# Kernel optimization log

Hardware: AMD Instinct MI355X
Metric: run time of the kernel (lower is better)

## Reference

```python
import jax, jax.numpy as jnp
import numpy as np

NUM_GENES = 50000
NUM_EDGES = 5000
NNZ = 1_600_000
NUM_PATHWAYS = 500
NUM_TREATMENTS = 20
D = 128        # embed_dim
LATENT = 128   # latent_dim
B, M = 64, 200


def setup_inputs() -> dict:
    key = jax.random.key(0)
    ks = jax.random.split(key, 14)
    gene_ids = jax.random.randint(ks[0], (B, M), 0, NUM_GENES)
    context_ids = jax.random.randint(ks[1], (B,), 0, NUM_TREATMENTS)
    # sparse incidence H (COO): H[row, col] = val, shape [NUM_GENES, NUM_EDGES]
    H_rows = jax.random.randint(ks[2], (NNZ,), 0, NUM_GENES)
    H_cols = jax.random.randint(ks[3], (NNZ,), 0, NUM_EDGES)
    H_vals = jnp.ones((NNZ,), jnp.float32)
    gene_embed = 0.02 * jax.random.normal(ks[4], (NUM_GENES, D), jnp.float32)
    treatment_embed = 0.02 * jax.random.normal(ks[5], (NUM_TREATMENTS, D), jnp.float32)
    gene_pathway = jax.random.bernoulli(ks[6], 0.05, (NUM_GENES, NUM_PATHWAYS)).astype(jnp.float32)
    s = 1.0 / np.sqrt(2 * D)
    W1 = s * jax.random.normal(ks[7], (2 * D, D), jnp.float32)
    b1 = jnp.zeros((D,), jnp.float32)
    W2 = (1.0 / np.sqrt(D)) * jax.random.normal(ks[8], (D,), jnp.float32)
    b2 = jnp.zeros((), jnp.float32)
    latent_W = (1.0 / np.sqrt(D)) * jax.random.normal(ks[9], (D, LATENT), jnp.float32)
    latent_b = jnp.zeros((LATENT,), jnp.float32)
    risk_W = (1.0 / np.sqrt(LATENT)) * jax.random.normal(ks[10], (LATENT,), jnp.float32)
    risk_b = jnp.zeros((), jnp.float32)
    return dict(gene_ids=gene_ids, context_ids=context_ids, H_rows=H_rows, H_cols=H_cols,
                H_vals=H_vals, gene_embed=gene_embed, treatment_embed=treatment_embed,
                gene_pathway=gene_pathway, W1=W1, b1=b1, W2=W2, b2=b2,
                latent_W=latent_W, latent_b=latent_b, risk_W=risk_W, risk_b=risk_b)


def _hyper_prop(E, H_rows, H_cols, H_vals):
    Dv = jax.ops.segment_sum(H_vals, H_rows, num_segments=NUM_GENES)
    De = jax.ops.segment_sum(H_vals, H_cols, num_segments=NUM_EDGES)
    dv = jnp.power(Dv + 1e-6, -0.5)[:, None]   # [V,1]
    de = jnp.power(De + 1e-6, -1.0)[:, None]   # [E,1]
    X = E * dv
    # H^T X : scatter node rows into hyperedges
    HX = jax.ops.segment_sum(H_vals[:, None] * X[H_rows], H_cols, num_segments=NUM_EDGES)
    HX = HX * de
    # H (De^-1 H^T X)
    Xp = jax.ops.segment_sum(H_vals[:, None] * HX[H_cols], H_rows, num_segments=NUM_GENES)
    return Xp * dv


def reference(gene_ids, context_ids, H_rows, H_cols, H_vals, gene_embed, treatment_embed,
              gene_pathway, W1, b1, W2, b2, latent_W, latent_b, risk_W, risk_b):
    E_prop = _hyper_prop(gene_embed, H_rows, H_cols, H_vals)   # [V,D]
    X = E_prop[gene_ids]                                       # [B,M,D]
    ctx = treatment_embed[context_ids]                         # [B,D]
    masks = gene_pathway[gene_ids]                             # [B,M,P]
    pathway_sum = jnp.einsum('bmd,bmp->bpd', X, masks)         # [B,P,D]
    counts = jnp.clip(masks.sum(axis=1), 1.0)[..., None]       # [B,P,1]
    rep = pathway_sum / counts                                 # [B,P,D]
    ctx_exp = jnp.broadcast_to(ctx[:, None, :], (rep.shape[0], NUM_PATHWAYS, D))
    attn_in = jnp.concatenate([rep, ctx_exp], axis=-1)         # [B,P,2D]
    h = jnp.tanh(attn_in @ W1 + b1)                            # [B,P,D]
    scores = h @ W2 + b2                                       # [B,P]
    w = jax.nn.softmax(scores, axis=-1)
    z0 = jnp.einsum('bp,bpd->bd', w, rep)                      # [B,D]
    z = z0 @ latent_W + latent_b                               # [B,LATENT]
    risk = z @ risk_W + risk_b                                 # [B]
    return risk, z
```

## Files before the change

### kernel.cpp

```cpp
#include <hip/hip_runtime.h>
#include <math.h>

#define NGENES 50000
#define NEDGES 5000
#define NNZ_C 1600000
#define NPATH 500
#define DIM 128
#define BB 64
#define MM 200
#define BMN (BB * MM)
#define NBMW 1568
#define CSRCAP 400000
#define NCH 128
#define CHUNK (NNZ_C / NCH)
#define RNG 12512
#define GSTRIDE 50048
#define NT 8
#define TILESZ 6250
#define NBIN (NT * NEDGES)
#define BIN0 50048
#define RED_N 90048
#define SCB_BIN 40
#define SCB_ROW 49
#define SCB (SCB_BIN + SCB_ROW)


__device__ inline float wred_sum(float x) {
#pragma unroll
  for (int off = 32; off > 0; off >>= 1) x += __shfl_down(x, off, 64);
  return x;
}
__device__ inline int wred_sumi(int x) {
#pragma unroll
  for (int off = 32; off > 0; off >>= 1) x += __shfl_down(x, off, 64);
  return x;
}
__device__ inline float wred_max(float x) {
#pragma unroll
  for (int off = 32; off > 0; off >>= 1) x = fmaxf(x, __shfl_down(x, off, 64));
  return x;
}
__device__ inline int wave_incl_scan(int x) {
  int lane = threadIdx.x & 63;
#pragma unroll
  for (int off = 1; off < 64; off <<= 1) {
    int y = __shfl_up(x, off, 64);
    if (lane >= off) x += y;
  }
  return x;
}

__global__ void k_mark(const int* __restrict__ gene_ids, unsigned* __restrict__ bitmap) {
  int i = blockIdx.x * blockDim.x + threadIdx.x;
  if (i >= BMN) return;
  int g = gene_ids[i];
  atomicOr(bitmap + (g >> 5), 1u << (g & 31));
}

__global__ void k_build(const int* __restrict__ rows, const int* __restrict__ cols,
                        unsigned char* __restrict__ pgc, unsigned char* __restrict__ pbc) {
  __shared__ int hs[RNG];
  int c = blockIdx.x, role = blockIdx.y, tid = threadIdx.x;
  int lo = c * CHUNK, hi = lo + CHUNK;
  if (role == 0) {
    for (int j = tid; j < RNG; j += 1024) hs[j] = 0;
    __syncthreads();
    for (int i = lo + tid; i < hi; i += 1024) {
      int r = rows[i];
      int k = r / RNG;
      int j = r - k * RNG;
      atomicAdd(&hs[j], 1 << (k * 8));
    }
    __syncthreads();
    unsigned char* dst = pgc + (size_t)c * GSTRIDE;
    for (int j = tid; j < RNG; j += 1024) {
      unsigned v = (unsigned)hs[j];
      dst[j] = (unsigned char)(v & 0xFFu);
      dst[j + RNG] = (unsigned char)((v >> 8) & 0xFFu);
      dst[j + 2 * RNG] = (unsigned char)((v >> 16) & 0xFFu);
      dst[j + 3 * RNG] = (unsigned char)(v >> 24);
    }
  } else {
    for (int j = tid; j < 2 * NEDGES; j += 1024) hs[j] = 0;
    __syncthreads();
    for (int i = lo + tid; i < hi; i += 1024) {
      int r = rows[i];
      int t = r / TILESZ;
      int e = cols[i];
      atomicAdd(&hs[(t >> 2) * NEDGES + e], 1 << ((t & 3) * 8));
    }
    __syncthreads();
    unsigned char* dst = pbc + (size_t)c * NBIN;
    for (int j = tid; j < 2 * NEDGES; j += 1024) {
      int h = j / NEDGES, e = j - h * NEDGES;
      unsigned v = (unsigned)hs[j];
      int t0 = h * 4;
      dst[(size_t)(t0 + 0) * NEDGES + e] = (unsigned char)(v & 0xFFu);
      dst[(size_t)(t0 + 1) * NEDGES + e] = (unsigned char)((v >> 8) & 0xFFu);
      dst[(size_t)(t0 + 2) * NEDGES + e] = (unsigned char)((v >> 16) & 0xFFu);
      dst[(size_t)(t0 + 3) * NEDGES + e] = (unsigned char)(v >> 24);
    }
  }
}

__global__ void k_reduce(const unsigned char* __restrict__ pgc,
                         const unsigned char* __restrict__ pbc,
                         const unsigned* __restrict__ bitmap,
                         float* __restrict__ dv_inv, int* __restrict__ row_cnt,
                         unsigned short* __restrict__ ccpre8, int* __restrict__ cnt8em) {
  int idx = blockIdx.x * 256 + threadIdx.x;
  if (idx < NGENES) {
    int s = 0;
    for (int c = 0; c < NCH; ++c) s += pgc[(size_t)c * GSTRIDE + idx];
    dv_inv[idx] = 1.f / sqrtf((float)s + 1e-6f);
    row_cnt[idx] = ((bitmap[idx >> 5] >> (idx & 31)) & 1) ? s : 0;
  } else if (idx >= BIN0 && idx < BIN0 + NBIN) {
    int b = idx - BIN0;
    int t = b / NEDGES, e = b - t * NEDGES;
    int run = 0;
    for (int c = 0; c < NCH; ++c) {
      ccpre8[(size_t)c * NBIN + b] = (unsigned short)run;
      run += pbc[(size_t)c * NBIN + b];
    }
    cnt8em[(e << 3) | t] = run;
  }
}

__global__ void k_sc1(const int* __restrict__ cnt8em, const int* __restrict__ row_cnt,
                      int* __restrict__ bsum) {
  __shared__ int wsum[4];
  int blk = blockIdx.x, t = threadIdx.x, lane = t & 63, wid = t >> 6;
  const int* in;
  int base, n;
  if (blk < SCB_BIN) { in = cnt8em; base = blk * 1024; n = NBIN; }
  else { in = row_cnt; base = (blk - SCB_BIN) * 1024; n = NGENES; }
  int s = 0;
#pragma unroll
  for (int k = 0; k < 4; ++k) {
    int e = base + t + k * 256;
    if (e < n) s += in[e];
  }
  s = wred_sumi(s);
  if (lane == 0) wsum[wid] = s;
  __syncthreads();
  if (t == 0) bsum[blk] = wsum[0] + wsum[1] + wsum[2] + wsum[3];
}

__global__ void k_sc2(const int* __restrict__ bsum, int* __restrict__ boff) {
  int t = threadIdx.x, lane = t & 63, wid = t >> 6;
  if (wid == 0) {
    int x = (lane < SCB_BIN) ? bsum[lane] : 0;
    int incl = wave_incl_scan(x);
    if (lane < SCB_BIN) boff[lane] = incl - x;
  } else {
    int x = (lane < SCB_ROW) ? bsum[SCB_BIN + lane] : 0;
    int incl = wave_incl_scan(x);
    if (lane < SCB_ROW) boff[SCB_BIN + lane] = incl - x;
  }
}

__global__ void k_sc3(const int* __restrict__ cnt8em, const int* __restrict__ row_cnt,
                      const int* __restrict__ boff,
                      int* __restrict__ start8, int* __restrict__ row_start,
                      float* __restrict__ de_inv) {
  __shared__ int lds[1024];
  __shared__ int wsum[4];
  int blk = blockIdx.x, t = threadIdx.x, lane = t & 63, wid = t >> 6;
  const int* in;
  int* out;
  int base, n;
  if (blk < SCB_BIN) { in = cnt8em; out = start8; base = blk * 1024; n = NBIN; }
  else { in = row_cnt; out = row_start; base = (blk - SCB_BIN) * 1024; n = NGENES; }
  int coff = boff[blk];
#pragma unroll
  for (int k = 0; k < 4; ++k) {
    int e = t + k * 256;
    lds[e] = (base + e < n) ? in[base + e] : 0;
  }
  __syncthreads();
  int x0 = lds[4 * t], x1 = lds[4 * t + 1], x2 = lds[4 * t + 2], x3 = lds[4 * t + 3];
  int s = x0 + x1 + x2 + x3;
  int incl = wave_incl_scan(s);
  if (lane == 63) wsum[wid] = incl;
  __syncthreads();
  int woff = 0;
  for (int w = 0; w < wid; ++w) woff += wsum[w];
  int tb = coff + woff + incl - s;
  int i0 = base + 4 * t;
  if (i0 + 3 < n) {
    ((int4*)(out + i0))[0] = make_int4(tb, tb + x0, tb + x0 + x1, tb + x0 + x1 + x2);
  } else {
    if (i0 < n) out[i0] = tb;
    if (i0 + 1 < n) out[i0 + 1] = tb + x0;
    if (i0 + 2 < n) out[i0 + 2] = tb + x0 + x1;
    if (i0 + 3 < n) out[i0 + 3] = tb + x0 + x1 + x2;
  }
  if (blk < SCB_BIN && t < 128) {
    int e = blk * 128 + t;
    if (e < NEDGES) {
      int s8 = 0;
#pragma unroll
      for (int u = 0; u < 8; ++u) s8 += lds[8 * t + u];
      de_inv[e] = 1.f / ((float)s8 + 1e-6f);
    }
  }
}

__global__ void k_place(const int* __restrict__ rows, const int* __restrict__ cols,
                        const int* __restrict__ start8, const unsigned short* __restrict__ ccpre8,
                        const int* __restrict__ row_start, int* __restrict__ row_cur,
                        const unsigned* __restrict__ bitmap,
                        unsigned short* __restrict__ csc, unsigned short* __restrict__ csr) {
  __shared__ int cnt_s[NEDGES];
  __shared__ unsigned bm_s[NBMW];
  int c = blockIdx.x, q = blockIdx.y, tid = threadIdx.x;
  int lo = c * CHUNK, hi = lo + CHUNK;
  for (int j = tid; j < NEDGES; j += 1024) cnt_s[j] = 0;
  for (int j = tid; j < NBMW; j += 1024) bm_s[j] = bitmap[j];
  __syncthreads();
  const unsigned short* cp = ccpre8 + (size_t)c * NBIN;
  int qlo = q * (4 * TILESZ);
  for (int i = lo + tid; i < hi; i += 1024) {
    int r = rows[i];
    unsigned d = (unsigned)(r - qlo);
    if (d >= 4u * TILESZ) continue;
    int e = cols[i];
    int tt = (int)(d / (unsigned)TILESZ);
    int t = 4 * q + tt;
    int sh = tt * 8;
    int old = atomicAdd(&cnt_s[e], 1 << sh);
    int rank = (old >> sh) & 0xFF;
    int pos = start8[e * 8 + t] + (int)cp[(size_t)t * NEDGES + e] + rank;
    csc[pos] = (unsigned short)(d - (unsigned)(tt * TILESZ));
    if ((bm_s[r >> 5] >> (r & 31)) & 1) {
      int p2 = row_start[r] + atomicAdd(row_cur + r, 1);
      if (p2 < CSRCAP) csr[p2] = (unsigned short)e;
    }
  }
}

__global__ void k_edge_t(const int* __restrict__ start8, const int* __restrict__ cnt8em,
                         const unsigned short* __restrict__ csc,
                         const float* __restrict__ dv_inv, const float* __restrict__ ge,
                         float* __restrict__ part) {
  __shared__ float4 red[32];
  int bid = blockIdx.x;
  int s = start8[bid];
  int n = cnt8em[bid];
  int rbase = (bid & 7) * TILESZ;
  int g = threadIdx.x >> 5, l = threadIdx.x & 31;
  float4 a0 = make_float4(0.f, 0.f, 0.f, 0.f);
  float4 a1 = make_float4(0.f, 0.f, 0.f, 0.f);
  float4 a2 = make_float4(0.f, 0.f, 0.f, 0.f);
  float4 a3 = make_float4(0.f, 0.f, 0.f, 0.f);
  int i = s + g;
  int end = s + n;
  unsigned short c0 = 0, c1 = 0, c2 = 0, c3 = 0, c4 = 0, c5 = 0, c6 = 0, c7 = 0;
  bool have = (i + 14 < end);
  if (have) {
    c0 = csc[i];      c1 = csc[i + 2];  c2 = csc[i + 4];  c3 = csc[i + 6];
    c4 = csc[i + 8];  c5 = csc[i + 10]; c6 = csc[i + 12]; c7 = csc[i + 14];
  }
  while (have) {
    int ni = i + 16;
    bool nhave = (ni + 14 < end);
    unsigned short n0 = c0, n1 = c1, n2 = c2, n3 = c3, n4 = c4, n5 = c5, n6 = c6, n7 = c7;
    if (nhave) {
      n0 = csc[ni];      n1 = csc[ni + 2];  n2 = csc[ni + 4];  n3 = csc[ni + 6];
      n4 = csc[ni + 8];  n5 = csc[ni + 10]; n6 = csc[ni + 12]; n7 = csc[ni + 14];
    }
    int r0 = rbase + c0, r1 = rbase + c1, r2 = rbase + c2, r3 = rbase + c3;
    int r4 = rbase + c4, r5 = rbase + c5, r6 = rbase + c6, r7 = rbase + c7;
    float w0 = dv_inv[r0], w1 = dv_inv[r1], w2 = dv_inv[r2], w3 = dv_inv[r3];
    float w4 = dv_inv[r4], w5 = dv_inv[r5], w6 = dv_inv[r6], w7 = dv_inv[r7];
    float4 x0 = *((const float4*)(ge + (size_t)r0 * DIM) + l);
    float4 x1 = *((const float4*)(ge + (size_t)r1 * DIM) + l);
    float4 x2 = *((const float4*)(ge + (size_t)r2 * DIM) + l);
    float4 x3 = *((const float4*)(ge + (size_t)r3 * DIM) + l);
    float4 x4 = *((const float4*)(ge + (size_t)r4 * DIM) + l);
    float4 x5 = *((const float4*)(ge + (size_t)r5 * DIM) + l);
    float4 x6 = *((const float4*)(ge + (size_t)r6 * DIM) + l);
    float4 x7 = *((const float4*)(ge + (size_t)r7 * DIM) + l);
    a0.x += w0 * x0.x; a0.y += w0 * x0.y; a0.z += w0 * x0.z; a0.w += w0 * x0.w;
    a1.x += w1 * x1.x; a1.y += w1 * x1.y; a1.z += w1 * x1.z; a1.w += w1 * x1.w;
    a2.x += w2 * x2.x; a2.y += w2 * x2.y; a2.z += w2 * x2.z; a2.w += w2 * x2.w;
    a3.x += w3 * x3.x; a3.y += w3 * x3.y; a3.z += w3 * x3.z; a3.w += w3 * x3.w;
    a0.x += w4 * x4.x; a0.y += w4 * x4.y; a0.z += w4 * x4.z; a0.w += w4 * x4.w;
    a1.x += w5 * x5.x; a1.y += w5 * x5.y; a1.z += w5 * x5.z; a1.w += w5 * x5.w;
    a2.x += w6 * x6.x; a2.y += w6 * x6.y; a2.z += w6 * x6.z; a2.w += w6 * x6.w;
    a3.x += w7 * x7.x; a3.y += w7 * x7.y; a3.z += w7 * x7.z; a3.w += w7 * x7.w;
    c0 = n0; c1 = n1; c2 = n2; c3 = n3; c4 = n4; c5 = n5; c6 = n6; c7 = n7;
    i = ni;
    have = nhave;
  }
  for (; i + 2 < end; i += 4) {
    int ra = rbase + csc[i], rb = rbase + csc[i + 2];
    float wa = dv_inv[ra], wb = dv_inv[rb];
    float4 xa = *((const float4*)(ge + (size_t)ra * DIM) + l);
    float4 xb = *((const float4*)(ge + (size_t)rb * DIM) + l);
    a0.x += wa * xa.x; a0.y += wa * xa.y; a0.z += wa * xa.z; a0.w += wa * xa.w;
    a1.x += wb * xb.x; a1.y += wb * xb.y; a1.z += wb * xb.z; a1.w += wb * xb.w;
  }
  for (; i < end; i += 2) {
    int r = rbase + csc[i];
    float w = dv_inv[r];
    float4 x = *((const float4*)(ge + (size_t)r * DIM) + l);
    a0.x += w * x.x; a0.y += w * x.y; a0.z += w * x.z; a0.w += w * x.w;
  }
  a0.x += a1.x + a2.x + a3.x;
  a0.y += a1.y + a2.y + a3.y;
  a0.z += a1.z + a2.z + a3.z;
  a0.w += a1.w + a2.w + a3.w;
  if (g == 1) red[l] = a0;
  __syncthreads();
  if (g == 0) {
    float4 b = red[l];
    a0.x += b.x; a0.y += b.y; a0.z += b.z; a0.w += b.w;
    *((float4*)(part + (size_t)bid * DIM) + l) = a0;
  }
}

__global__ void k_edge_red(const float* __restrict__ part, const float* __restrict__ de_inv,
                           float* __restrict__ HXde) {
  int e = blockIdx.x, d = threadIdx.x;
  float s = 0.f;
#pragma unroll
  for (int t = 0; t < NT; ++t) s += part[((size_t)e * 8 + t) * DIM + d];
  HXde[(size_t)e * DIM + d] = s * de_inv[e];
}

__global__ void k_gene(const int* __restrict__ gene_ids, const int* __restrict__ row_start,
                       const int* __restrict__ row_cnt, const unsigned short* __restrict__ csr,
                       const float* __restrict__ HXde, const float* __restrict__ dv_inv,
                       float* __restrict__ Xg) {
  __shared__ float4 red[4][32];
  int bm = blockIdx.x;
  int gene = gene_ids[bm];
  int s = row_start[gene], n = row_cnt[gene];
  int end = s + n;
  int g = threadIdx.x >> 5, l = threadIdx.x & 31;
  float4 a0 = make_float4(0.f, 0.f, 0.f, 0.f);
  float4 a1 = make_float4(0.f, 0.f, 0.f, 0.f);
  int i = s + g;
  for (; i + 12 < end; i += 16) {
    int e0 = csr[i];
    int e1 = csr[i + 4];
    int e2 = csr[i + 8];
    int e3 = csr[i + 12];
    float4 x0 = *((const float4*)(HXde + (size_t)e0 * DIM) + l);
    float4 x1 = *((const float4*)(HXde + (size_t)e1 * DIM) + l);
    float4 x2 = *((const float4*)(HXde + (size_t)e2 * DIM) + l);
    float4 x3 = *((const float4*)(HXde + (size_t)e3 * DIM) + l);
    a0.x += x0.x; a0.y += x0.y; a0.z += x0.z; a0.w += x0.w;
    a1.x += x1.x; a1.y += x1.y; a1.z += x1.z; a1.w += x1.w;
    a0.x += x2.x; a0.y += x2.y; a0.z += x2.z; a0.w += x2.w;
    a1.x += x3.x; a1.y += x3.y; a1.z += x3.z; a1.w += x3.w;
  }
  for (; i + 4 < end; i += 8) {
    int e0 = csr[i];
    int e1 = csr[i + 4];
    float4 x0 = *((const float4*)(HXde + (size_t)e0 * DIM) + l);
    float4 x1 = *((const float4*)(HXde + (size_t)e1 * DIM) + l);
    a0.x += x0.x; a0.y += x0.y; a0.z += x0.z; a0.w += x0.w;
    a1.x += x1.x; a1.y += x1.y; a1.z += x1.z; a1.w += x1.w;
  }
  for (; i < end; i += 4) {
    int e0 = csr[i];
    float4 x = *((const float4*)(HXde + (size_t)e0 * DIM) + l);
    a0.x += x.x; a0.y += x.y; a0.z += x.z; a0.w += x.w;
  }
  a0.x += a1.x; a0.y += a1.y; a0.z += a1.z; a0.w += a1.w;
  red[g][l] = a0;
  __syncthreads();
  if (g == 0) {
    float4 a = red[0][l], b = red[1][l], c = red[2][l], d = red[3][l];
    float dvg = dv_inv[gene];
    float4 o;
    o.x = (a.x + b.x + c.x + d.x) * dvg;
    o.y = (a.y + b.y + c.y + d.y) * dvg;
    o.z = (a.z + b.z + c.z + d.z) * dvg;
    o.w = (a.w + b.w + c.w + d.w) * dvg;
    *((float4*)(Xg + (size_t)bm * DIM) + l) = o;
  }
}

#define PT 20
#define CHM 25
__global__ void k_pathway(const int* __restrict__ gene_ids,
                          const float* __restrict__ gene_pathway,
                          const float* __restrict__ Xg, float* __restrict__ rep) {
  __shared__ __align__(16) float buf[2][CHM * PT];
  __shared__ int gid_s[MM];
  int b = blockIdx.y;
  int p0 = blockIdx.x * PT;
  int t = threadIdx.x;
  int d = t;
  if (t < 128) gid_s[t] = gene_ids[b * MM + t];
  if (t + 128 < MM) gid_s[t + 128] = gene_ids[b * MM + t + 128];
  __syncthreads();
  float acc[PT], cnt[PT];
#pragma unroll
  for (int pp = 0; pp < PT; ++pp) { acc[pp] = 0.f; cnt[pp] = 0.f; }
  float r[4];
#pragma unroll
  for (int k = 0; k < 4; ++k) {
    int e = t + k * 128;
    if (e < CHM * PT) {
      int ml = e / PT, po = e - ml * PT;
      r[k] = gene_pathway[(size_t)gid_s[ml] * NPATH + p0 + po];
    }
  }
  const float* Xb = Xg + (size_t)b * MM * DIM + d;
  for (int ch = 0; ch < MM / CHM; ++ch) {
    float* bw = buf[ch & 1];
#pragma unroll
    for (int k = 0; k < 4; ++k) {
      int e = t + k * 128;
      if (e < CHM * PT) bw[e] = r[k];
    }
    __syncthreads();
    if (ch + 1 < MM / CHM) {
      int m0n = (ch + 1) * CHM;
#pragma unroll
      for (int k = 0; k < 4; ++k) {
        int e = t + k * 128;
        if (e < CHM * PT) {
          int ml = e / PT, po = e - ml * PT;
          r[k] = gene_pathway[(size_t)gid_s[m0n + ml] * NPATH + p0 + po];
        }
      }
    }
    const float* br = buf[ch & 1];
    int m0 = ch * CHM;
    for (int ml = 0; ml < CHM; ++ml) {
      float x = Xb[(size_t)(m0 + ml) * DIM];
      const float4* mr = (const float4*)(br + ml * PT);
#pragma unroll
      for (int q = 0; q < 5; ++q) {
        float4 v = mr[q];
        acc[4 * q + 0] += v.x * x; cnt[4 * q + 0] += v.x;
        acc[4 * q + 1] += v.y * x; cnt[4 * q + 1] += v.y;
        acc[4 * q + 2] += v.z * x; cnt[4 * q + 2] += v.z;
        acc[4 * q + 3] += v.w * x; cnt[4 * q + 3] += v.w;
      }
    }
  }
#pragma unroll
  for (int pp = 0; pp < PT; ++pp) {
    rep[((size_t)b * NPATH + p0 + pp) * DIM + d] = acc[pp] / fmaxf(cnt[pp], 1.f);
  }
}

#define PT2 10
__global__ void k_attn(const float* __restrict__ rep, const int* __restrict__ context_ids,
                       const float* __restrict__ treatment_embed,
                       const float* __restrict__ W1, const float* __restrict__ b1,
                       const float* __restrict__ W2, const float* __restrict__ b2,
                       float* __restrict__ scores) {
  __shared__ float in_s[PT2][DIM];
  __shared__ float ctx_s[DIM];
  __shared__ float part[PT2][2];
  int b = blockIdx.y;
  int p0 = blockIdx.x * PT2;
  int j = threadIdx.x;
  int lane = j & 63, wid = j >> 6;
  ctx_s[j] = treatment_embed[context_ids[b] * DIM + j];
#pragma unroll
  for (int pp = 0; pp < PT2; ++pp)
    in_s[pp][j] = rep[((size_t)b * NPATH + p0 + pp) * DIM + j];
  __syncthreads();
  float base = b1[j];
  for (int k = 0; k < DIM; ++k) base += ctx_s[k] * W1[(DIM + k) * DIM + j];
  float acc[PT2];
#pragma unroll
  for (int pp = 0; pp < PT2; ++pp) acc[pp] = base;
  for (int k = 0; k < DIM; ++k) {
    float w1 = W1[k * DIM + j];
#pragma unroll
    for (int pp = 0; pp < PT2; ++pp) acc[pp] += in_s[pp][k] * w1;
  }
  float w2 = W2[j];
#pragma unroll
  for (int pp = 0; pp < PT2; ++pp) {
    float t = tanhf(acc[pp]) * w2;
    t = wred_sum(t);
    if (lane == 0) part[pp][wid] = t;
  }
  __syncthreads();
  if (j < PT2) scores[b * NPATH + p0 + j] = part[j][0] + part[j][1] + b2[0];
}

__global__ void k_final(const float* __restrict__ scores, const float* __restrict__ rep,
                        const float* __restrict__ latent_W, const float* __restrict__ latent_b,
                        const float* __restrict__ risk_W, const float* __restrict__ risk_b,
                        float* __restrict__ out) {
  __shared__ float w_s[NPATH];
  __shared__ float z0_s[DIM];
  __shared__ float red_max[2], red_sum[2], red_risk[2];
  int b = blockIdx.x, t = threadIdx.x;
  int lane = t & 63, wid = t >> 6;
  float lmax = -3.4e38f;
  for (int p = t; p < NPATH; p += 128) {
    float s = scores[b * NPATH + p];
    w_s[p] = s;
    lmax = fmaxf(lmax, s);
  }
  lmax = wred_max(lmax);
  if (lane == 0) red_max[wid] = lmax;
  __syncthreads();
  float bmax = fmaxf(red_max[0], red_max[1]);
  float lsum = 0.f;
  for (int p = t; p < NPATH; p += 128) {
    float e = expf(w_s[p] - bmax);
    w_s[p] = e;
    lsum += e;
  }
  lsum = wred_sum(lsum);
  if (lane == 0) red_sum[wid] = lsum;
  __syncthreads();
  float inv = 1.f / (red_sum[0] + red_sum[1]);
  int d = t;
  const float* repb = rep + (size_t)b * NPATH * DIM + d;
  float z00 = 0.f, z01 = 0.f, z02 = 0.f, z03 = 0.f;
  for (int p = 0; p < NPATH; p += 4) {
    z00 += w_s[p] * repb[(size_t)p * DIM];
    z01 += w_s[p + 1] * repb[(size_t)(p + 1) * DIM];
    z02 += w_s[p + 2] * repb[(size_t)(p + 2) * DIM];
    z03 += w_s[p + 3] * repb[(size_t)(p + 3) * DIM];
  }
  float z0 = ((z00 + z01) + (z02 + z03)) * inv;
  z0_s[d] = z0;
  __syncthreads();
  float z = latent_b[t];
  for (int dd = 0; dd < DIM; ++dd) z += z0_s[dd] * latent_W[dd * DIM + t];
  out[BB + b * DIM + t] = z;
  float r = z * risk_W[t];
  r = wred_sum(r);
  if (lane == 0) red_risk[wid] = r;
  __syncthreads();
  if (t == 0) out[b] = red_risk[0] + red_risk[1] + risk_b[0];
}

extern "C" void kernel_launch(void* const* d_in, const int* in_sizes, int n_in,
                              void* d_out, int out_size, void* d_ws, size_t ws_size,
                              hipStream_t stream) {
  const int* gene_ids = (const int*)d_in[0];
  const int* context_ids = (const int*)d_in[1];
  const int* H_rows = (const int*)d_in[2];
  const int* H_cols = (const int*)d_in[3];
  const float* gene_embed = (const float*)d_in[5];
  const float* treatment_embed = (const float*)d_in[6];
  const float* gene_pathway = (const float*)d_in[7];
  const float* W1 = (const float*)d_in[8];
  const float* b1 = (const float*)d_in[9];
  const float* W2 = (const float*)d_in[10];
  const float* b2 = (const float*)d_in[11];
  const float* latent_W = (const float*)d_in[12];
  const float* latent_b = (const float*)d_in[13];
  const float* risk_W = (const float*)d_in[14];
  const float* risk_b = (const float*)d_in[15];
  float* out = (float*)d_out;

  char* ws = (char*)d_ws;
  float* dv_inv = (float*)(ws + 0);
  float* de_inv = (float*)(ws + 200000);
  int* row_cnt = (int*)(ws + 220000);
  int* row_start = (int*)(ws + 420000);
  int* cnt8em = (int*)(ws + 620000);
  int* start8 = (int*)(ws + 780000);
  float* scores = (float*)(ws + 940000);
  int* bsum = (int*)(ws + 1068032);
  int* boff = (int*)(ws + 1068544);
  int* row_cur = (int*)(ws + 1069056);
  unsigned* bitmap = (unsigned*)(ws + 1269056);
  unsigned short* ccpre8 = (unsigned short*)(ws + 1275328);
  unsigned char* pgc = (unsigned char*)(ws + 11515328);
  unsigned char* pbc = (unsigned char*)(ws + 17921472);
  unsigned short* csc = (unsigned short*)(ws + 11515328);
  unsigned short* csr = (unsigned short*)(ws + 14715328);
  float* part = (float*)(ws + 15515328);
  float* HXde = (float*)(ws + 11515328);
  float* Xg = (float*)(ws + 15515328);
  float* rep = (float*)(ws + 22068928);

  hipMemsetAsync(ws + 1069056, 0, 206272, stream);

  k_mark<<<(BMN + 255) / 256, 256, 0, stream>>>(gene_ids, bitmap);
  k_build<<<dim3(NCH, 2), 1024, 0, stream>>>(H_rows, H_cols, pgc, pbc);
  k_reduce<<<(RED_N + 255) / 256, 256, 0, stream>>>(pgc, pbc, bitmap, dv_inv, row_cnt,
                                                    ccpre8, cnt8em);
  k_sc1<<<SCB, 256, 0, stream>>>(cnt8em, row_cnt, bsum);
  k_sc2<<<1, 128, 0, stream>>>(bsum, boff);
  k_sc3<<<SCB, 256, 0, stream>>>(cnt8em, row_cnt, boff, start8, row_start, de_inv);
  k_place<<<dim3(NCH, 2), 1024, 0, stream>>>(H_rows, H_cols, start8, ccpre8,
                                             row_start, row_cur, bitmap, csc, csr);
  k_edge_t<<<NBIN, 64, 0, stream>>>(start8, cnt8em, csc, dv_inv, gene_embed, part);
  k_edge_red<<<NEDGES, DIM, 0, stream>>>(part, de_inv, HXde);
  k_gene<<<BMN, 128, 0, stream>>>(gene_ids, row_start, row_cnt, csr, HXde, dv_inv, Xg);
  k_pathway<<<dim3(NPATH / PT, BB), DIM, 0, stream>>>(gene_ids, gene_pathway, Xg, rep);
  k_attn<<<dim3(NPATH / PT2, BB), DIM, 0, stream>>>(rep, context_ids, treatment_embed,
                                                    W1, b1, W2, b2, scores);
  k_final<<<BB, DIM, 0, stream>>>(scores, rep, latent_W, latent_b, risk_W, risk_b, out);
}
```

Before: 413.4 us.

## Pack COO histograms into 4-bit nibbles with finer chunks and single-role blocks

The gene-degree and edge/tile histograms are now packed at 4 bits per count, with 8 genes or 8 tiles per 32-bit word, and the number of NNZ chunks is doubled to 256. Each block builds both histograms in one pass instead of being split into role-specific blocks, and k_place handles all tiles in one pass instead of two row-range passes. The per-chunk prefix table shrinks from 16-bit to 8-bit entries, and its layout changes to edge-major so lookups index by e*8+t. The aim is to cut rereads of rows/cols and the byte traffic of the intermediate count arrays. The cost is that counts must fit in 4 bits per chunk (6250 entries per chunk), which can overflow for unlucky distributions and carry into the neighbouring nibble.

```diff
diff --git a/kernel.cpp b/kernel.cpp
--- a/kernel.cpp
+++ b/kernel.cpp
@@ -11,10 +11,9 @@
 #define BMN (BB * MM)
 #define NBMW 1568
 #define CSRCAP 400000
-#define NCH 128
+#define NCH 256
 #define CHUNK (NNZ_C / NCH)
-#define RNG 12512
-#define GSTRIDE 50048
+#define GW 6250
 #define NT 8
 #define TILESZ 6250
 #define NBIN (NT * NEDGES)
@@ -58,71 +57,49 @@
 }
 
 __global__ void k_build(const int* __restrict__ rows, const int* __restrict__ cols,
-                        unsigned char* __restrict__ pgc, unsigned char* __restrict__ pbc) {
-  __shared__ int hs[RNG];
-  int c = blockIdx.x, role = blockIdx.y, tid = threadIdx.x;
+                        unsigned* __restrict__ pgc, unsigned* __restrict__ pbc) {
+  __shared__ int hg[GW];
+  __shared__ int hb[NEDGES];
+  int c = blockIdx.x, tid = threadIdx.x;
   int lo = c * CHUNK, hi = lo + CHUNK;
-  if (role == 0) {
-    for (int j = tid; j < RNG; j += 1024) hs[j] = 0;
-    __syncthreads();
-    for (int i = lo + tid; i < hi; i += 1024) {
-      int r = rows[i];
-      int k = r / RNG;
-      int j = r - k * RNG;
-      atomicAdd(&hs[j], 1 << (k * 8));
-    }
-    __syncthreads();
-    unsigned char* dst = pgc + (size_t)c * GSTRIDE;
-    for (int j = tid; j < RNG; j += 1024) {
-      unsigned v = (unsigned)hs[j];
-      dst[j] = (unsigned char)(v & 0xFFu);
-      dst[j + RNG] = (unsigned char)((v >> 8) & 0xFFu);
-      dst[j + 2 * RNG] = (unsigned char)((v >> 16) & 0xFFu);
-      dst[j + 3 * RNG] = (unsigned char)(v >> 24);
-    }
-  } else {
-    for (int j = tid; j < 2 * NEDGES; j += 1024) hs[j] = 0;
-    __syncthreads();
-    for (int i = lo + tid; i < hi; i += 1024) {
-      int r = rows[i];
-      int t = r / TILESZ;
-      int e = cols[i];
-      atomicAdd(&hs[(t >> 2) * NEDGES + e], 1 << ((t & 3) * 8));
-    }
-    __syncthreads();
-    unsigned char* dst = pbc + (size_t)c * NBIN;
-    for (int j = tid; j < 2 * NEDGES; j += 1024) {
-      int h = j / NEDGES, e = j - h * NEDGES;
-      unsigned v = (unsigned)hs[j];
-      int t0 = h * 4;
-      dst[(size_t)(t0 + 0) * NEDGES + e] = (unsigned char)(v & 0xFFu);
-      dst[(size_t)(t0 + 1) * NEDGES + e] = (unsigned char)((v >> 8) & 0xFFu);
-      dst[(size_t)(t0 + 2) * NEDGES + e] = (unsigned char)((v >> 16) & 0xFFu);
-      dst[(size_t)(t0 + 3) * NEDGES + e] = (unsigned char)(v >> 24);
-    }
-  }
-}
-
-__global__ void k_reduce(const unsigned char* __restrict__ pgc,
-                         const unsigned char* __restrict__ pbc,
+  for (int j = tid; j < GW; j += 1024) hg[j] = 0;
+  for (int j = tid; j < NEDGES; j += 1024) hb[j] = 0;
+  __syncthreads();
+  for (int i = lo + tid; i < hi; i += 1024) {
+    int r = rows[i];
+    int e = cols[i];
+    atomicAdd(&hg[r >> 3], 1 << ((r & 7) * 4));
+    int t = r / TILESZ;
+    atomicAdd(&hb[e], 1 << (t * 4));
+  }
+  __syncthreads();
+  unsigned* dg = pgc + (size_t)c * GW;
+  for (int j = tid; j < GW; j += 1024) dg[j] = (unsigned)hg[j];
+  unsigned* db = pbc + (size_t)c * NEDGES;
+  for (int j = tid; j < NEDGES; j += 1024) db[j] = (unsigned)hb[j];
+}
+
+__global__ void k_reduce(const unsigned* __restrict__ pgc,
+                         const unsigned* __restrict__ pbc,
                          const unsigned* __restrict__ bitmap,
                          float* __restrict__ dv_inv, int* __restrict__ row_cnt,
-                         unsigned short* __restrict__ ccpre8, int* __restrict__ cnt8em) {
+                         unsigned char* __restrict__ ccpre8, int* __restrict__ cnt8em) {
   int idx = blockIdx.x * 256 + threadIdx.x;
   if (idx < NGENES) {
+    int w = idx >> 3, f = (idx & 7) * 4;
     int s = 0;
-    for (int c = 0; c < NCH; ++c) s += pgc[(size_t)c * GSTRIDE + idx];
+    for (int c = 0; c < NCH; ++c) s += (pgc[(size_t)c * GW + w] >> f) & 0xF;
     dv_inv[idx] = 1.f / sqrtf((float)s + 1e-6f);
     row_cnt[idx] = ((bitmap[idx >> 5] >> (idx & 31)) & 1) ? s : 0;
   } else if (idx >= BIN0 && idx < BIN0 + NBIN) {
     int b = idx - BIN0;
-    int t = b / NEDGES, e = b - t * NEDGES;
+    int e = b >> 3, f = (b & 7) * 4;
     int run = 0;
     for (int c = 0; c < NCH; ++c) {
-      ccpre8[(size_t)c * NBIN + b] = (unsigned short)run;
-      run += pbc[(size_t)c * NBIN + b];
-    }
-    cnt8em[(e << 3) | t] = run;
+      ccpre8[(size_t)c * NBIN + b] = (unsigned char)run;
+      run += (pbc[(size_t)c * NEDGES + e] >> f) & 0xF;
+    }
+    cnt8em[b] = run;
   }
 }
 
@@ -207,31 +184,28 @@
 }
 
 __global__ void k_place(const int* __restrict__ rows, const int* __restrict__ cols,
-                        const int* __restrict__ start8, const unsigned short* __restrict__ ccpre8,
+                        const int* __restrict__ start8, const unsigned char* __restrict__ ccpre8,
                         const int* __restrict__ row_start, int* __restrict__ row_cur,
                         const unsigned* __restrict__ bitmap,
                         unsigned short* __restrict__ csc, unsigned short* __restrict__ csr) {
   __shared__ int cnt_s[NEDGES];
   __shared__ unsigned bm_s[NBMW];
-  int c = blockIdx.x, q = blockIdx.y, tid = threadIdx.x;
+  int c = blockIdx.x, tid = threadIdx.x;
   int lo = c * CHUNK, hi = lo + CHUNK;
   for (int j = tid; j < NEDGES; j += 1024) cnt_s[j] = 0;
   for (int j = tid; j < NBMW; j += 1024) bm_s[j] = bitmap[j];
   __syncthreads();
-  const unsigned short* cp = ccpre8 + (size_t)c * NBIN;
-  int qlo = q * (4 * TILESZ);
+  const unsigned char* cp = ccpre8 + (size_t)c * NBIN;
   for (int i = lo + tid; i < hi; i += 1024) {
     int r = rows[i];
-    unsigned d = (unsigned)(r - qlo);
-    if (d >= 4u * TILESZ) continue;
     int e = cols[i];
-    int tt = (int)(d / (unsigned)TILESZ);
-    int t = 4 * q + tt;
-    int sh = tt * 8;
+    int t = r / TILESZ;
+    int sh = t * 4;
     int old = atomicAdd(&cnt_s[e], 1 << sh);
-    int rank = (old >> sh) & 0xFF;
-    int pos = start8[e * 8 + t] + (int)cp[(size_t)t * NEDGES + e] + rank;
-    csc[pos] = (unsigned short)(d - (unsigned)(tt * TILESZ));
+    int rank = (old >> sh) & 0xF;
+    int b = e * 8 + t;
+    int pos = start8[b] + (int)cp[b] + rank;
+    csc[pos] = (unsigned short)(r - t * TILESZ);
     if ((bm_s[r >> 5] >> (r & 31)) & 1) {
       int p2 = row_start[r] + atomicAdd(row_cur + r, 1);
       if (p2 < CSRCAP) csr[p2] = (unsigned short)e;
@@ -573,9 +547,9 @@
   int* boff = (int*)(ws + 1068544);
   int* row_cur = (int*)(ws + 1069056);
   unsigned* bitmap = (unsigned*)(ws + 1269056);
-  unsigned short* ccpre8 = (unsigned short*)(ws + 1275328);
-  unsigned char* pgc = (unsigned char*)(ws + 11515328);
-  unsigned char* pbc = (unsigned char*)(ws + 17921472);
+  unsigned char* ccpre8 = (unsigned char*)(ws + 1275328);
+  unsigned* pgc = (unsigned*)(ws + 11515328);
+  unsigned* pbc = (unsigned*)(ws + 17915328);
   unsigned short* csc = (unsigned short*)(ws + 11515328);
   unsigned short* csr = (unsigned short*)(ws + 14715328);
   float* part = (float*)(ws + 15515328);
@@ -586,14 +560,14 @@
   hipMemsetAsync(ws + 1069056, 0, 206272, stream);
 
   k_mark<<<(BMN + 255) / 256, 256, 0, stream>>>(gene_ids, bitmap);
-  k_build<<<dim3(NCH, 2), 1024, 0, stream>>>(H_rows, H_cols, pgc, pbc);
+  k_build<<<NCH, 1024, 0, stream>>>(H_rows, H_cols, pgc, pbc);
   k_reduce<<<(RED_N + 255) / 256, 256, 0, stream>>>(pgc, pbc, bitmap, dv_inv, row_cnt,
                                                     ccpre8, cnt8em);
   k_sc1<<<SCB, 256, 0, stream>>>(cnt8em, row_cnt, bsum);
   k_sc2<<<1, 128, 0, stream>>>(bsum, boff);
   k_sc3<<<SCB, 256, 0, stream>>>(cnt8em, row_cnt, boff, start8, row_start, de_inv);
-  k_place<<<dim3(NCH, 2), 1024, 0, stream>>>(H_rows, H_cols, start8, ccpre8,
-                                             row_start, row_cur, bitmap, csc, csr);
+  k_place<<<NCH, 1024, 0, stream>>>(H_rows, H_cols, start8, ccpre8,
+                                    row_start, row_cur, bitmap, csc, csr);
   k_edge_t<<<NBIN, 64, 0, stream>>>(start8, cnt8em, csc, dv_inv, gene_embed, part);
   k_edge_red<<<NEDGES, DIM, 0, stream>>>(part, de_inv, HXde);
   k_gene<<<BMN, 128, 0, stream>>>(gene_ids, row_start, row_cnt, csr, HXde, dv_inv, Xg);
```

Result: slower. 425.1 us (+2.8%).
